# Kernel optimization log

Hardware: AMD Instinct MI355X
Metric: run time of the kernel (lower is better)

The kernel has to match this reference:

```python
import jax, jax.numpy as jnp
import numpy as np

H, W = 1024, 1024
NUM_FEATURES = 64
NUM_PILLARS = 100000


def setup_inputs() -> dict:
    key = jax.random.key(0)
    k1, k2 = jax.random.split(key)
    pillar_features = jax.random.normal(k1, (NUM_PILLARS, NUM_FEATURES), dtype=jnp.float32)
    coords = jax.random.randint(k2, (NUM_PILLARS, 3), 0, 1024, dtype=jnp.int64)
    return {"pillar_features": pillar_features, "coords": coords}


def reference(pillar_features, coords):
    # pillar_features: [N, F]; coords: [N, 3] = (batch_idx, y_idx, x_idx)
    x_idx = coords[:, 2]
    y_idx = coords[:, 1]
    valid = (x_idx >= 0) & (x_idx < W) & (y_idx >= 0) & (y_idx < H)
    # Flatten spatial dims; route invalid pillars to an out-of-bounds slot
    # that mode='drop' discards (matches the torch valid_mask filtering).
    flat_idx = jnp.where(valid, y_idx * W + x_idx, H * W)
    img = jnp.zeros((NUM_FEATURES, H * W), dtype=pillar_features.dtype)
    # single vectorized scatter: [F, N] updates into [F, H*W]
    img = img.at[:, flat_idx].set(pillar_features.T, mode='drop')
    return img.reshape(1, NUM_FEATURES, H, W)
```

## Files before the change

### kernel.cpp

```cpp
#include <hip/hip_runtime.h>


constexpr int H  = 1024;
constexpr int W  = 1024;
constexpr int HW = H * W;
constexpr int NF = 64;
constexpr int TILE = 64;
constexpr int LSTR = NF + 1;

__global__ void winner_kernel(const int* __restrict__ coords,
                              int* __restrict__ winner, int np) {
    int p = blockIdx.x * blockDim.x + threadIdx.x;
    if (p >= np) return;
    int y = coords[p * 3 + 1];
    int x = coords[p * 3 + 2];
    if ((unsigned)x < (unsigned)W && (unsigned)y < (unsigned)H) {
        atomicMax(winner + (y * W + x), p);
    }
}

__global__ void __launch_bounds__(256) fill_kernel(const float* __restrict__ feat,
                                                   const int* __restrict__ winner,
                                                   float* __restrict__ out) {
    __shared__ float lds[TILE * LSTR];
    __shared__ int   wc[TILE];

    const int base = blockIdx.x * TILE;
    const int t    = threadIdx.x;

    if (t < TILE) wc[t] = winner[base + t];
    __syncthreads();

    {
        const int c  = t >> 2;
        const int j  = t & 3;
        const int wp = wc[c];
        float* dst = lds + c * LSTR + j * 16;
        if (wp >= 0) {
            const float4* row = (const float4*)(feat + (size_t)wp * NF) + j * 4;
            float4 a = row[0], b = row[1], cc = row[2], d = row[3];
            dst[0]=a.x; dst[1]=a.y; dst[2]=a.z; dst[3]=a.w;
            dst[4]=b.x; dst[5]=b.y; dst[6]=b.z; dst[7]=b.w;
            dst[8]=cc.x; dst[9]=cc.y; dst[10]=cc.z; dst[11]=cc.w;
            dst[12]=d.x; dst[13]=d.y; dst[14]=d.z; dst[15]=d.w;
        } else {
#pragma unroll
            for (int k = 0; k < 16; ++k) dst[k] = 0.0f;
        }
    }
    __syncthreads();

    {
        const int f0 = t >> 4;
        const int cg = t & 15;
#pragma unroll
        for (int iter = 0; iter < 4; ++iter) {
            const int f = iter * 16 + f0;
            float4 v;
            v.x = lds[(cg * 4 + 0) * LSTR + f];
            v.y = lds[(cg * 4 + 1) * LSTR + f];
            v.z = lds[(cg * 4 + 2) * LSTR + f];
            v.w = lds[(cg * 4 + 3) * LSTR + f];
            *(float4*)(out + (size_t)f * HW + base + cg * 4) = v;
        }
    }
}

extern "C" void kernel_launch(void* const* d_in, const int* in_sizes, int n_in,
                              void* d_out, int out_size, void* d_ws, size_t ws_size,
                              hipStream_t stream) {
    const float* feat   = (const float*)d_in[0];
    const int*   coords = (const int*)d_in[1];
    float*       out    = (float*)d_out;
    int np = in_sizes[1] / 3;

    int* winner = (int*)d_ws;

    hipMemsetAsync(winner, 0xFF, (size_t)HW * sizeof(int), stream);
    winner_kernel<<<(np + 255) / 256, 256, 0, stream>>>(coords, winner, np);
    fill_kernel<<<HW / TILE, 256, 0, stream>>>(feat, winner, out);
}
```

Baseline: 306.9 us.

## Restructure fill kernel: 256-cell tiles, feature-major LDS, two halves, nontemporal stores

Each thread now owns one output cell and writes that pillar's features into a feature-major LDS layout. This removes the padded transpose and gives contiguous 1KB rows per feature. The tile grows from 64 to 256 cells and the 64 features are processed in two halves of 32 to bound LDS use. Output writes use nontemporal stores so the 256MB image does not pollute cache. The cost is an extra barrier pair per half, plus strided per-thread global reads of feature rows.

```diff
diff --git a/kernel.cpp b/kernel.cpp
--- a/kernel.cpp
+++ b/kernel.cpp
@@ -1,12 +1,14 @@
 #include <hip/hip_runtime.h>
 
 
-constexpr int H  = 1024;
-constexpr int W  = 1024;
-constexpr int HW = H * W;
-constexpr int NF = 64;
-constexpr int TILE = 64;
-constexpr int LSTR = NF + 1;
+constexpr int H    = 1024;
+constexpr int W    = 1024;
+constexpr int HW   = H * W;
+constexpr int NF   = 64;
+constexpr int TILE = 256;
+constexpr int HALF = 32;
+
+typedef float nt4 __attribute__((ext_vector_type(4)));
 
 __global__ void winner_kernel(const int* __restrict__ coords,
                               int* __restrict__ winner, int np) {
@@ -22,47 +24,41 @@
 __global__ void __launch_bounds__(256) fill_kernel(const float* __restrict__ feat,
                                                    const int* __restrict__ winner,
                                                    float* __restrict__ out) {
-    __shared__ float lds[TILE * LSTR];
-    __shared__ int   wc[TILE];
+    __shared__ float lds[HALF * TILE];
 
     const int base = blockIdx.x * TILE;
     const int t    = threadIdx.x;
+    const int wp   = winner[base + t];
+    const int wv   = t >> 6;
+    const int l    = t & 63;
 
-    if (t < TILE) wc[t] = winner[base + t];
-    __syncthreads();
+    const float4* row = (const float4*)(feat + (size_t)max(wp, 0) * NF);
 
-    {
-        const int c  = t >> 2;
-        const int j  = t & 3;
-        const int wp = wc[c];
-        float* dst = lds + c * LSTR + j * 16;
+#pragma unroll
+    for (int h = 0; h < 2; ++h) {
         if (wp >= 0) {
-            const float4* row = (const float4*)(feat + (size_t)wp * NF) + j * 4;
-            float4 a = row[0], b = row[1], cc = row[2], d = row[3];
-            dst[0]=a.x; dst[1]=a.y; dst[2]=a.z; dst[3]=a.w;
-            dst[4]=b.x; dst[5]=b.y; dst[6]=b.z; dst[7]=b.w;
-            dst[8]=cc.x; dst[9]=cc.y; dst[10]=cc.z; dst[11]=cc.w;
-            dst[12]=d.x; dst[13]=d.y; dst[14]=d.z; dst[15]=d.w;
+#pragma unroll
+            for (int j = 0; j < 8; ++j) {
+                float4 r = row[h * 8 + j];
+                lds[(j * 4 + 0) * TILE + t] = r.x;
+                lds[(j * 4 + 1) * TILE + t] = r.y;
+                lds[(j * 4 + 2) * TILE + t] = r.z;
+                lds[(j * 4 + 3) * TILE + t] = r.w;
+            }
         } else {
 #pragma unroll
-            for (int k = 0; k < 16; ++k) dst[k] = 0.0f;
+            for (int j = 0; j < HALF; ++j) lds[j * TILE + t] = 0.0f;
         }
-    }
-    __syncthreads();
+        __syncthreads();
 
-    {
-        const int f0 = t >> 4;
-        const int cg = t & 15;
 #pragma unroll
-        for (int iter = 0; iter < 4; ++iter) {
-            const int f = iter * 16 + f0;
-            float4 v;
-            v.x = lds[(cg * 4 + 0) * LSTR + f];
-            v.y = lds[(cg * 4 + 1) * LSTR + f];
-            v.z = lds[(cg * 4 + 2) * LSTR + f];
-            v.w = lds[(cg * 4 + 3) * LSTR + f];
-            *(float4*)(out + (size_t)f * HW + base + cg * 4) = v;
+        for (int p = 0; p < 8; ++p) {
+            const int floc = p * 4 + wv;
+            nt4 v = *(const nt4*)&lds[floc * TILE + l * 4];
+            __builtin_nontemporal_store(
+                v, (nt4*)(out + (size_t)(h * HALF + floc) * HW + base + l * 4));
         }
+        __syncthreads();
     }
 }
 
@@ -76,7 +72,7 @@
 
     int* winner = (int*)d_ws;
 
-    hipMemsetAsync(winner, 0xFF, (size_t)HW * sizeof(int), stream);
+    (void)hipMemsetAsync(winner, 0xFF, (size_t)HW * sizeof(int), stream);
     winner_kernel<<<(np + 255) / 256, 256, 0, stream>>>(coords, winner, np);
     fill_kernel<<<HW / TILE, 256, 0, stream>>>(feat, winner, out);
 }
```

New measurement: 297.9 us. -2.9%, faster.
